# Performance work log

Measured on AMD Instinct MI355X. Metric: run time of the kernel, lower is better.

Reference implementation:

```python
import jax, jax.numpy as jnp
import numpy as np

N = 2_000_000
IN_DIM = 1
HID = 64
NUM_SEG = 2048


def setup_inputs() -> dict:
    key = jax.random.key(0)
    ks = jax.random.split(key, 8)
    x = jax.random.normal(ks[0], (N, IN_DIM), dtype=jnp.float32)
    batch = jnp.sort(jax.random.randint(ks[1], (N,), 0, NUM_SEG, dtype=jnp.int64))
    s1 = 1.0 / np.sqrt(IN_DIM)
    s2 = 1.0 / np.sqrt(HID)
    W1 = jax.random.uniform(ks[2], (HID, IN_DIM), jnp.float32, -s1, s1)
    b1 = jax.random.uniform(ks[3], (HID,), jnp.float32, -s1, s1)
    W2 = jax.random.uniform(ks[4], (HID, HID), jnp.float32, -s2, s2)
    b2 = jax.random.uniform(ks[5], (HID,), jnp.float32, -s2, s2)
    W3 = jax.random.uniform(ks[6], (1, HID), jnp.float32, -s2, s2)
    b3 = jax.random.uniform(ks[7], (1,), jnp.float32, -s2, s2)
    return {"x": x, "batch": batch, "W1": W1, "b1": b1, "W2": W2, "b2": b2, "W3": W3, "b3": b3}


def reference(x, batch, W1, b1, W2, b2, W3, b3):
    batch = batch.astype(jnp.int32)
    h = jax.nn.relu(x @ W1.T + b1)          # [N, HID]
    h = jax.nn.relu(h @ W2.T + b2)          # [N, HID]
    pooled = jax.ops.segment_sum(h, batch, num_segments=NUM_SEG)  # [NUM_SEG, HID]
    counts = jax.ops.segment_sum(jnp.ones((h.shape[0],), h.dtype), batch, num_segments=NUM_SEG)
    pooled = pooled / jnp.maximum(counts, 1.0)[:, None]  # segment mean
    weights = jax.nn.relu((pooled @ W3.T + b3)[:, 0])    # [NUM_SEG]
    return weights[batch]                    # broadcast back to points [N]
```

## Files before the change

kernel.cpp:

```cpp
#include <hip/hip_runtime.h>
#include <math.h>

#define NSEG 2048
#define ROW 65
#define MMAX 4226
#define TCAP 4240
#define NC 4096
#define GLO (-9.0f)
#define GHI (9.0f)
#define DXF ((GHI - GLO) / NC)
#define INVDX (NC / (GHI - GLO))
#define SCAN_PPT 8

__global__ __launch_bounds__(256) void k_pre_scan(
    const float* __restrict__ W1, const float* __restrict__ b1,
    const float* __restrict__ W2, const float* __restrict__ b2,
    const float* __restrict__ W3, const int* __restrict__ batch,
    float* __restrict__ bpg, float* __restrict__ knots, float2* __restrict__ coef,
    int* __restrict__ nvalid, int* __restrict__ seg_start, int* __restrict__ seg_end,
    int n)
{
    __shared__ float bps[64];
    __shared__ float w2s[64 * 65];
    __shared__ float sc_[64], sda[64], sdb[64];
    const int tid = threadIdx.x;

    if (blockIdx.x >= 65) {
        int bid2 = blockIdx.x - 65;
        int base = bid2 * (256 * SCAN_PPT) + tid * SCAN_PPT;
        if (base >= n) return;
        const int4* bp = (const int4*)(batch + base);
        int4 a4 = bp[0], b4 = bp[1];
        int ss[SCAN_PPT] = {a4.x, a4.y, a4.z, a4.w, b4.x, b4.y, b4.z, b4.w};
        int prev = (base > 0) ? batch[base - 1] : -1;
#pragma unroll
        for (int p = 0; p < SCAN_PPT; ++p) {
            int u = (p == 0) ? prev : ss[p - 1];
            int v = ss[p];
            if (v != u) {
                int i = base + p;
                for (int s = (u > 0 ? u : 0); s < v; ++s) seg_end[s] = i;
                for (int s = u + 1; s <= v; ++s) seg_start[s] = i;
            }
        }
        if (base + SCAN_PPT >= n) {
            int u = ss[SCAN_PPT - 1];
            for (int s = u; s < NSEG; ++s) seg_end[s] = n;
            for (int s = u + 1; s < NSEG; ++s) seg_start[s] = n;
        }
        return;
    }

    const int k = blockIdx.x;
    const int lane = tid & 63;

    if (tid < 64) {
        float w1l = W1[lane], b1l = b1[lane];
        float t = (w1l != 0.0f) ? (-b1l / w1l) : 3.0e38f;
        int r = 0;
        for (int l = 0; l < 64; ++l) {
            float o = __shfl(t, l);
            r += (o < t) || (o == t && l < lane);
        }
        bps[r] = t;
    }
    for (int i = tid; i < 4096; i += 256)
        w2s[(i >> 6) * 65 + (i & 63)] = W2[i];
    __syncthreads();
    if (k == 0 && tid < 64) bpg[lane] = bps[lane];

    float a0 = 0.0f, b0 = 0.0f;
    if (tid < 64) {
        float lof = (k == 0) ? (bps[0] - 1.0f) : bps[k - 1];
        float hif = (k == 64) ? (bps[63] + 1.0f) : bps[k];
        float xm = lof + 0.5f * (hif - lof);
        float a = 0.0f, b = b2[lane];
        for (int j = 0; j < 64; ++j) {
            float w1 = W1[j];
            if (w1 * xm + b1[j] > 0.0f) {
                float w2 = w2s[lane * 65 + j];
                a += w2 * w1;
                b += w2 * b1[j];
            }
        }

        float w3 = W3[lane];
        float lo = (k == 0) ? -INFINITY : bps[k - 1];
        float hi = (k == 64) ? INFINITY : bps[k];
        float c = INFINITY, da = 0.0f, db = 0.0f;
        if (a != 0.0f) {
            float cc = -b / a;
            if (cc > lo && cc < hi) {
                float s = (a > 0.0f) ? 1.0f : -1.0f;
                c = cc; da = s * w3 * a; db = s * w3 * b;
            }
        }
        bool act;
        if (k == 0) act = (a < 0.0f) || (a == 0.0f && b > 0.0f);
        else { float v = a * lo + b; act = (v > 0.0f) || (v == 0.0f && a > 0.0f); }
        a0 = act ? w3 * a : 0.0f;
        b0 = act ? w3 * b : 0.0f;
        for (int d = 32; d; d >>= 1) { a0 += __shfl_xor(a0, d); b0 += __shfl_xor(b0, d); }

        int rank = 0;
        for (int l = 0; l < 64; ++l) {
            float o = __shfl(c, l);
            rank += (o < c) || (o == c && l < lane);
        }
        sc_[rank] = c; sda[rank] = da; sdb[rank] = db;
    }
    __syncthreads();
    if (tid < 64) {
        float cs = sc_[lane], das = sda[lane], dbs = sdb[lane];
        for (int d = 1; d < 64; d <<= 1) {
            float ta = __shfl_up(das, d);
            float tb = __shfl_up(dbs, d);
            if (lane >= d) { das += ta; dbs += tb; }
        }
        knots[k * ROW + lane] = cs;
        if (lane == 0) coef[k * ROW] = make_float2(a0, b0);
        coef[k * ROW + lane + 1] = make_float2(a0 + das, b0 + dbs);

        unsigned long long vm = __ballot(isfinite(cs));
        if (lane == 0) nvalid[k] = (int)__popcll(vm);
    }
}

__global__ __launch_bounds__(64) void k_pre_c2(
    const float* __restrict__ bpg, const int* __restrict__ nvalid,
    const float* __restrict__ knots2d, const float2* __restrict__ coef2d,
    float* __restrict__ Tf, float2* __restrict__ Cf,
    unsigned short* __restrict__ baseg, int* __restrict__ Mg)
{
    const int lane = threadIdx.x;
    const int k = blockIdx.x;
    __shared__ float bps[64];
    __shared__ float trow[64];

    bps[lane] = bpg[lane];
    trow[lane] = knots2d[k * ROW + lane];

    int v = nvalid[lane] + 1;
    int sc = v;
    for (int d = 1; d < 64; d <<= 1) {
        int tt = __shfl_up(sc, d);
        if (lane >= d) sc += tt;
    }
    const int offk  = (k == 0) ? 0 : __shfl(sc, k - 1);
    const int off64 = __shfl(sc, 63);
    const int nv    = nvalid[k];
    __syncthreads();

    for (int j = lane; j <= nv; j += 64) {
        if (j < nv) Tf[offk + j] = trow[j];
        else if (k < 64) Tf[offk + j] = bps[k];
        Cf[offk + j] = coef2d[k * ROW + j];
    }
    if (k == 64) {
        const int M = off64 + nvalid[64];
        float2 lastC = coef2d[64 * ROW + nvalid[64]];
        for (int i = M + lane; i < TCAP; i += 64) Tf[i] = INFINITY;
        for (int i = M + 1 + lane; i < MMAX; i += 64) Cf[i] = lastC;
        if (lane == 0) Mg[0] = M;
    }

    float lob = (k == 0) ? GLO : bps[k - 1];
    float hib = (k == 64) ? GHI : bps[k];
    float clo = fminf(fmaxf((lob - GLO) * INVDX, 0.0f), (float)(NC - 1));
    float chi = fminf(fmaxf((hib - GLO) * INVDX, 0.0f), (float)(NC - 1));
    int c0 = max(0, (int)clo - 1);
    int c1 = min(NC - 1, (int)chi + 1);
    for (int c = c0 + lane; c <= c1; c += 64) {
        float left = GLO + c * DXF;
        bool ok = (k == 0 || left >= bps[k - 1]) && (k == 64 || left < bps[k]);
        if (ok) {
            int j = 0;
#pragma unroll
            for (int ofs = 32; ofs >= 1; ofs >>= 1)
                if (trow[j + ofs - 1] <= left) j += ofs;
            if (j < 64 && trow[j] <= left) ++j;
            baseg[c] = (unsigned short)(offk + j);
        }
    }
}

__global__ __launch_bounds__(256) void k_eval_out(
    const float* __restrict__ x,
    const int* __restrict__ seg_start, const int* __restrict__ seg_end,
    const float* __restrict__ Tf, const float2* __restrict__ Cf,
    const unsigned short* __restrict__ baseg, const int* __restrict__ Mg,
    const float* __restrict__ b3, float* __restrict__ out)
{
    __shared__ __align__(16) float T_s[TCAP];
    __shared__ double wsum[4];
    __shared__ float w_s;
    const int tid = threadIdx.x;
    const int s = blockIdx.x;

    const int start = seg_start[s];
    const int end   = seg_end[s];

    const int stageN = min(TCAP, (Mg[0] + 32) & ~15);
    for (int i = tid; i < (stageN >> 2); i += 256)
        ((float4*)T_s)[i] = ((const float4*)Tf)[i];
    __syncthreads();
    if (start >= end) return;

    double acc = 0.0;
    for (int i = start + tid; i < end; i += 256) {
        float xv = x[i];
        int m;
        if (xv >= GLO) {
            int c = (int)((xv - GLO) * INVDX);
            c = c < NC - 1 ? c : NC - 1;
            if (c > 0 && GLO + c * DXF > xv) --c;
            int b0i = baseg[c];
            int a0 = b0i & ~3;
            const float4* tw = (const float4*)(T_s + a0);
            float4 t0 = tw[0], t1 = tw[1], t2 = tw[2];
            int cw = (t0.x <= xv) + (t0.y <= xv) + (t0.z <= xv) + (t0.w <= xv)
                   + (t1.x <= xv) + (t1.y <= xv) + (t1.z <= xv) + (t1.w <= xv)
                   + (t2.x <= xv) + (t2.y <= xv) + (t2.z <= xv) + (t2.w <= xv);
            m = a0 + cw;
            if (cw == 12) { while (T_s[m] <= xv) ++m; }
        } else m = 0;
        float2 ab = Cf[m];
        acc += (double)fmaf(ab.x, xv, ab.y);
    }

    for (int d = 32; d; d >>= 1) acc += __shfl_down(acc, d);
    if ((tid & 63) == 0) wsum[tid >> 6] = acc;
    __syncthreads();
    if (tid == 0) {
        double tot = wsum[0] + wsum[1] + wsum[2] + wsum[3];
        double mean = tot / (double)(end - start);
        w_s = fmaxf((float)(mean + (double)b3[0]), 0.0f);
    }
    __syncthreads();
    const float w = w_s;
    for (int i = start + tid; i < end; i += 256) out[i] = w;
}

extern "C" void kernel_launch(void* const* d_in, const int* in_sizes, int n_in,
                              void* d_out, int out_size, void* d_ws, size_t ws_size,
                              hipStream_t stream)
{
    const float* x   = (const float*)d_in[0];
    const int* batch = (const int*)d_in[1];
    const float* W1 = (const float*)d_in[2];
    const float* b1 = (const float*)d_in[3];
    const float* W2 = (const float*)d_in[4];
    const float* b2 = (const float*)d_in[5];
    const float* W3 = (const float*)d_in[6];
    const float* b3 = (const float*)d_in[7];
    float* out = (float*)d_out;
    const int n = in_sizes[0];

    char* ws = (char*)d_ws;
    int*    seg_start= (int*)ws;
    int*    seg_end  = (int*)(ws + 8192);
    float*  bpg      = (float*)(ws + 16384);
    int*    nvalid   = (int*)(ws + 16640);
    int*    Mg       = (int*)(ws + 16912);
    float*  knots2d  = (float*)(ws + 16928);
    float2* coef2d   = (float2*)(ws + 33840);
    float*  Tflat    = (float*)(ws + 67648);
    float2* Cflat    = (float2*)(ws + 84608);
    unsigned short* baseg = (unsigned short*)(ws + 118416);

    const int scanBlocks = (n + 256 * SCAN_PPT - 1) / (256 * SCAN_PPT);
    k_pre_scan<<<65 + scanBlocks, 256, 0, stream>>>(
        W1, b1, W2, b2, W3, batch, bpg, knots2d, coef2d, nvalid,
        seg_start, seg_end, n);
    k_pre_c2<<<65, 64, 0, stream>>>(bpg, nvalid, knots2d, coef2d,
                                    Tflat, Cflat, baseg, Mg);
    k_eval_out<<<NSEG, 256, 0, stream>>>(x, seg_start, seg_end, Tflat, Cflat,
                                         baseg, Mg, b3, out);
}
```

Before: 30.23 us.

## Fuse piecewise-table assembly into precompute kernel via inter-block flags; stage baseg in LDS

```diff
diff --git a/kernel.cpp b/kernel.cpp
--- a/kernel.cpp
+++ b/kernel.cpp
@@ -2,7 +2,6 @@
 #include <math.h>
 
 #define NSEG 2048
-#define ROW 65
 #define MMAX 4226
 #define TCAP 4240
 #define NC 4096
@@ -11,18 +10,23 @@
 #define DXF ((GHI - GLO) / NC)
 #define INVDX (NC / (GHI - GLO))
 #define SCAN_PPT 8
-
-__global__ __launch_bounds__(256) void k_pre_scan(
+#define MAGIC 0x5EC7A100u
+
+__global__ __launch_bounds__(256) void k_pre(
     const float* __restrict__ W1, const float* __restrict__ b1,
     const float* __restrict__ W2, const float* __restrict__ b2,
     const float* __restrict__ W3, const int* __restrict__ batch,
-    float* __restrict__ bpg, float* __restrict__ knots, float2* __restrict__ coef,
-    int* __restrict__ nvalid, int* __restrict__ seg_start, int* __restrict__ seg_end,
-    int n)
+    unsigned int* __restrict__ nv_pub, int* __restrict__ Mg,
+    float* __restrict__ Tf, float2* __restrict__ Cf,
+    unsigned short* __restrict__ baseg,
+    int* __restrict__ seg_start, int* __restrict__ seg_end, int n)
 {
     __shared__ float bps[64];
     __shared__ float w2s[64 * 65];
-    __shared__ float sc_[64], sda[64], sdb[64];
+    __shared__ float cr_[64], sda[64], sdb[64];
+    __shared__ float ca_[65], cb_[65];
+    __shared__ int nvLDS[65];
+    __shared__ int off_s, M_s;
     const int tid = threadIdx.x;
 
     if (blockIdx.x >= 65) {
@@ -67,7 +71,6 @@
     for (int i = tid; i < 4096; i += 256)
         w2s[(i >> 6) * 65 + (i & 63)] = W2[i];
     __syncthreads();
-    if (k == 0 && tid < 64) bpg[lane] = bps[lane];
 
     float a0 = 0.0f, b0 = 0.0f;
     if (tid < 64) {
@@ -102,66 +105,69 @@
         b0 = act ? w3 * b : 0.0f;
         for (int d = 32; d; d >>= 1) { a0 += __shfl_xor(a0, d); b0 += __shfl_xor(b0, d); }
 
+        unsigned long long vm = __ballot(isfinite(c));
+        int nv = (int)__popcll(vm);
+        if (lane == 0)
+            __hip_atomic_store(&nv_pub[k], MAGIC | (unsigned)nv,
+                               __ATOMIC_RELEASE, __HIP_MEMORY_SCOPE_AGENT);
+
         int rank = 0;
         for (int l = 0; l < 64; ++l) {
             float o = __shfl(c, l);
             rank += (o < c) || (o == c && l < lane);
         }
-        sc_[rank] = c; sda[rank] = da; sdb[rank] = db;
-    }
-    __syncthreads();
-    if (tid < 64) {
-        float cs = sc_[lane], das = sda[lane], dbs = sdb[lane];
+        cr_[rank] = c; sda[rank] = da; sdb[rank] = db;
+    }
+    __syncthreads();
+    if (tid < 64) {
+        float das = sda[lane], dbs = sdb[lane];
         for (int d = 1; d < 64; d <<= 1) {
             float ta = __shfl_up(das, d);
             float tb = __shfl_up(dbs, d);
             if (lane >= d) { das += ta; dbs += tb; }
         }
-        knots[k * ROW + lane] = cs;
-        if (lane == 0) coef[k * ROW] = make_float2(a0, b0);
-        coef[k * ROW + lane + 1] = make_float2(a0 + das, b0 + dbs);
-
-        unsigned long long vm = __ballot(isfinite(cs));
-        if (lane == 0) nvalid[k] = (int)__popcll(vm);
-    }
-}
-
-__global__ __launch_bounds__(64) void k_pre_c2(
-    const float* __restrict__ bpg, const int* __restrict__ nvalid,
-    const float* __restrict__ knots2d, const float2* __restrict__ coef2d,
-    float* __restrict__ Tf, float2* __restrict__ Cf,
-    unsigned short* __restrict__ baseg, int* __restrict__ Mg)
-{
-    const int lane = threadIdx.x;
-    const int k = blockIdx.x;
-    __shared__ float bps[64];
-    __shared__ float trow[64];
-
-    bps[lane] = bpg[lane];
-    trow[lane] = knots2d[k * ROW + lane];
-
-    int v = nvalid[lane] + 1;
-    int sc = v;
-    for (int d = 1; d < 64; d <<= 1) {
-        int tt = __shfl_up(sc, d);
-        if (lane >= d) sc += tt;
-    }
-    const int offk  = (k == 0) ? 0 : __shfl(sc, k - 1);
-    const int off64 = __shfl(sc, 63);
-    const int nv    = nvalid[k];
-    __syncthreads();
-
-    for (int j = lane; j <= nv; j += 64) {
-        if (j < nv) Tf[offk + j] = trow[j];
+        if (lane == 0) { ca_[0] = a0; cb_[0] = b0; }
+        ca_[lane + 1] = a0 + das;
+        cb_[lane + 1] = b0 + dbs;
+    }
+
+    if (tid < 65) {
+        unsigned v;
+        for (;;) {
+            v = __hip_atomic_load(&nv_pub[tid], __ATOMIC_ACQUIRE,
+                                  __HIP_MEMORY_SCOPE_AGENT);
+            if ((v & 0xFFFFFF80u) == MAGIC) break;
+            __builtin_amdgcn_s_sleep(1);
+        }
+        nvLDS[tid] = (int)(v & 0x7Fu);
+    }
+    __syncthreads();
+    if (tid < 64) {
+        int v = nvLDS[lane] + 1;
+        int sc = v;
+        for (int d = 1; d < 64; d <<= 1) {
+            int tt = __shfl_up(sc, d);
+            if (lane >= d) sc += tt;
+        }
+        int offk  = (k == 0) ? 0 : __shfl(sc, k - 1);
+        int off64 = __shfl(sc, 63);
+        if (lane == 0) { off_s = offk; M_s = off64 + nvLDS[64]; }
+    }
+    __syncthreads();
+    const int offk = off_s;
+    const int M    = M_s;
+    const int nv   = nvLDS[k];
+
+    for (int j = tid; j <= nv; j += 256) {
+        if (j < nv) Tf[offk + j] = cr_[j];
         else if (k < 64) Tf[offk + j] = bps[k];
-        Cf[offk + j] = coef2d[k * ROW + j];
+        Cf[offk + j] = make_float2(ca_[j], cb_[j]);
     }
     if (k == 64) {
-        const int M = off64 + nvalid[64];
-        float2 lastC = coef2d[64 * ROW + nvalid[64]];
-        for (int i = M + lane; i < TCAP; i += 64) Tf[i] = INFINITY;
-        for (int i = M + 1 + lane; i < MMAX; i += 64) Cf[i] = lastC;
-        if (lane == 0) Mg[0] = M;
+        float2 lastC = make_float2(ca_[nv], cb_[nv]);
+        for (int i = M + tid; i < TCAP; i += 256) Tf[i] = INFINITY;
+        for (int i = M + 1 + tid; i < MMAX; i += 256) Cf[i] = lastC;
+        if (tid == 0) Mg[0] = M;
     }
 
     float lob = (k == 0) ? GLO : bps[k - 1];
@@ -170,15 +176,15 @@
     float chi = fminf(fmaxf((hib - GLO) * INVDX, 0.0f), (float)(NC - 1));
     int c0 = max(0, (int)clo - 1);
     int c1 = min(NC - 1, (int)chi + 1);
-    for (int c = c0 + lane; c <= c1; c += 64) {
+    for (int c = c0 + tid; c <= c1; c += 256) {
         float left = GLO + c * DXF;
         bool ok = (k == 0 || left >= bps[k - 1]) && (k == 64 || left < bps[k]);
         if (ok) {
             int j = 0;
 #pragma unroll
             for (int ofs = 32; ofs >= 1; ofs >>= 1)
-                if (trow[j + ofs - 1] <= left) j += ofs;
-            if (j < 64 && trow[j] <= left) ++j;
+                if (cr_[j + ofs - 1] <= left) j += ofs;
+            if (j < 64 && cr_[j] <= left) ++j;
             baseg[c] = (unsigned short)(offk + j);
         }
     }
@@ -192,17 +198,20 @@
     const float* __restrict__ b3, float* __restrict__ out)
 {
     __shared__ __align__(16) float T_s[TCAP];
+    __shared__ unsigned short base_s[NC];
     __shared__ double wsum[4];
     __shared__ float w_s;
     const int tid = threadIdx.x;
     const int s = blockIdx.x;
 
-    const int start = seg_start[s];
-    const int end   = seg_end[s];
-
     const int stageN = min(TCAP, (Mg[0] + 32) & ~15);
     for (int i = tid; i < (stageN >> 2); i += 256)
         ((float4*)T_s)[i] = ((const float4*)Tf)[i];
+    for (int i = tid; i < NC / 2; i += 256)
+        ((unsigned int*)base_s)[i] = ((const unsigned int*)baseg)[i];
+
+    const int start = seg_start[s];
+    const int end   = seg_end[s];
     __syncthreads();
     if (start >= end) return;
 
@@ -214,7 +223,7 @@
             int c = (int)((xv - GLO) * INVDX);
             c = c < NC - 1 ? c : NC - 1;
             if (c > 0 && GLO + c * DXF > xv) --c;
-            int b0i = baseg[c];
+            int b0i = base_s[c];
             int a0 = b0i & ~3;
             const float4* tw = (const float4*)(T_s + a0);
             float4 t0 = tw[0], t1 = tw[1], t2 = tw[2];
@@ -257,23 +266,18 @@
     const int n = in_sizes[0];
 
     char* ws = (char*)d_ws;
-    int*    seg_start= (int*)ws;
-    int*    seg_end  = (int*)(ws + 8192);
-    float*  bpg      = (float*)(ws + 16384);
-    int*    nvalid   = (int*)(ws + 16640);
-    int*    Mg       = (int*)(ws + 16912);
-    float*  knots2d  = (float*)(ws + 16928);
-    float2* coef2d   = (float2*)(ws + 33840);
-    float*  Tflat    = (float*)(ws + 67648);
-    float2* Cflat    = (float2*)(ws + 84608);
-    unsigned short* baseg = (unsigned short*)(ws + 118416);
+    int*    seg_start = (int*)ws;
+    int*    seg_end   = (int*)(ws + 8192);
+    unsigned int* nv_pub = (unsigned int*)(ws + 16384);
+    int*    Mg        = (int*)(ws + 16656);
+    float*  Tflat     = (float*)(ws + 16672);
+    float2* Cflat     = (float2*)(ws + 33632);
+    unsigned short* baseg = (unsigned short*)(ws + 67440);
 
     const int scanBlocks = (n + 256 * SCAN_PPT - 1) / (256 * SCAN_PPT);
-    k_pre_scan<<<65 + scanBlocks, 256, 0, stream>>>(
-        W1, b1, W2, b2, W3, batch, bpg, knots2d, coef2d, nvalid,
+    k_pre<<<65 + scanBlocks, 256, 0, stream>>>(
+        W1, b1, W2, b2, W3, batch, nv_pub, Mg, Tflat, Cflat, baseg,
         seg_start, seg_end, n);
-    k_pre_c2<<<65, 64, 0, stream>>>(bpg, nvalid, knots2d, coef2d,
-                                    Tflat, Cflat, baseg, Mg);
     k_eval_out<<<NSEG, 256, 0, stream>>>(x, seg_start, seg_end, Tflat, Cflat,
                                          baseg, Mg, b3, out);
 }
```

New measurement: 28.80 us. 1.05x faster.
